# Performance work log

Measured on AMD Instinct MI355X. Metric: run time of the kernel, lower is better.

The kernel has to match this reference:

```python
import jax, jax.numpy as jnp
import numpy as np

K = 3          # kernel_size (cubic)
S = 1          # stride
N_ITER = 3     # routing_iter
LAMBDA = 0.01  # inverse temperature used in M-step (CapsLayer default)
EPS = 1e-9


def _space_to_batch(x, k, s):
    # x: [B, D, H, W, C, ...] -> [B, oD, oH, oW, k^3 * C, ...]
    # patch ordering (kd, kh, kw, c) matches CapsLayer's gather+transpose+reshape.
    B, D, H, W, C = x.shape[:5]
    trail = x.shape[5:]
    oD = (D - k) // s + 1
    oH = (H - k) // s + 1
    oW = (W - k) // s + 1
    blocks = []
    for kd in range(k):
        for kh in range(k):
            for kw in range(k):
                blocks.append(x[:, kd:kd + oD * s:s, kh:kh + oH * s:s, kw:kw + oW * s:s])
    p = jnp.stack(blocks, axis=4)  # [B,oD,oH,oW,k^3,C,...]
    return p.reshape((B, oD, oH, oW, k ** 3 * C) + trail)


def _lse(x, axis):
    return jax.scipy.special.logsumexp(x, axis=axis, keepdims=True)


def _m_step(log_R, log_act, vote, bv, ba):
    # log_R: [...,I,O,1], log_act: [...,I,1,1], vote: [...,I,O,P]
    log_Ra = log_R + log_act
    R_sum = jnp.sum(jnp.exp(log_Ra), axis=-3, keepdims=True)        # [...,1,O,1]
    log_nR = log_Ra - _lse(log_Ra, axis=-3)                          # [...,I,O,1]
    pose = jnp.sum(vote * jnp.exp(log_nR), axis=-3, keepdims=True)   # [...,1,O,P]
    log_var = _lse(log_nR + jnp.log(jnp.square(vote - pose) + EPS), axis=-3)
    cost = R_sum * (bv + 0.5 * log_var)                              # [...,1,O,P]
    logit = LAMBDA * (ba - jnp.sum(cost, axis=-1, keepdims=True))    # [...,1,O,1]
    return pose, log_var, jax.nn.log_sigmoid(logit)


def _e_step(pose, log_var, log_act_out, vote):
    # per-dim Gaussian log-likelihood of votes under (pose, var)
    lp = -0.5 * (jnp.square(vote - pose) / jnp.exp(log_var) + log_var + jnp.log(2.0 * jnp.pi))
    lp = jnp.sum(lp, axis=-1, keepdims=True)                         # [...,I,O,1]
    logit = log_act_out + lp
    return logit - _lse(logit, axis=-2)                              # softmax over O


def _forward(pose, activation, W, beta_v, beta_a):
    pb = _space_to_batch(pose, K, S)            # [B,oD,oH,oW,I,4,4]
    ab = _space_to_batch(activation, K, S)      # [B,oD,oH,oW,I]
    # votes: W[i,o] @ pose_patch[...,i] -> [B,oD,oH,oW,I,O,4,4]
    vote = jnp.einsum('iork,bdhwikc->bdhwiorc', W, pb)
    vs = vote.shape
    vote = vote.reshape(vs[:-2] + (vs[-2] * vs[-1],))   # [...,I,O,16]
    nO = vote.shape[-2]
    log_act = jnp.log(ab + EPS)[..., None, None]        # [...,I,1,1]
    log_R = jnp.full(vote.shape[:-1] + (1,), -jnp.log(float(nO)), vote.dtype)
    bv = beta_v[None, None, None, None, None, :, :]     # [1,1,1,1,1,O,1]
    ba = beta_a[None, None, None, None, None, :, :]
    for t in range(N_ITER):
        v = vote if t == N_ITER - 1 else jax.lax.stop_gradient(vote)
        p, log_var, log_a = _m_step(log_R, log_act, v, bv, ba)
        if t < N_ITER - 1:
            log_R = _e_step(p, log_var, log_a, jax.lax.stop_gradient(vote))
    out_pose = jnp.squeeze(p, axis=-3).reshape(vs[:4] + (vs[-3], vs[-2], vs[-1]))  # [B,oD,oH,oW,O,4,4]
    out_act = jnp.exp(jnp.squeeze(log_a, axis=(-3, -1)))                            # [B,oD,oH,oW,O]
    return out_pose, out_act


def setup_inputs() -> dict:
    key = jax.random.key(0)
    k1, k2, k3, k4, k5 = jax.random.split(key, 5)
    pose = jax.random.normal(k1, (1, 12, 12, 12, 8, 4, 4), dtype=jnp.float32)
    activation = jax.random.uniform(k2, (1, 12, 12, 12, 8), dtype=jnp.float32)
    W = jax.random.normal(k3, (216, 16, 4, 4), dtype=jnp.float32)
    beta_v = jax.random.normal(k4, (16, 1), dtype=jnp.float32)
    beta_a = jax.random.normal(k5, (16, 1), dtype=jnp.float32)
    return {"pose": pose, "activation": activation, "W": W, "beta_v": beta_v, "beta_a": beta_a}


def reference(pose, activation, W, beta_v, beta_a):
    return _forward(pose, activation, W, beta_v, beta_a)
```

## Files before the change

kernel.cpp:

```cpp
#include <hip/hip_runtime.h>

#define NITER 3
#define LAMBDA 0.01f
#define EPS 1e-9f
#define LOG2PI 1.8378770664093453f

#define DIN 12
#define CIN 8
#define NI 216
#define NO 16
#define PPAD 20
#define RSTR 216

__global__ __launch_bounds__(512, 2)
void caps_em_kernel(const float* __restrict__ pose,
                    const float* __restrict__ act,
                    const float* __restrict__ W,
                    const float* __restrict__ beta_v,
                    const float* __restrict__ beta_a,
                    float* __restrict__ out)
{
    __shared__ __align__(16) float sPT[NI][PPAD];
    __shared__ __align__(16) float sRaT[NO][RSTR];
    __shared__ float sAct[NI];
    __shared__ __align__(16) float sPoseM[NO][16];
    __shared__ __align__(16) float sIvM[NO][16];
    __shared__ float sCo[NO];

    const int t = threadIdx.x;
    const int b = blockIdx.x;
    const int od = b / 100;
    const int rem = b - od * 100;
    const int oh = rem / 10;
    const int ow = rem - oh * 10;

    const int o = t >> 5;
    const int j = t & 31;

    for (int u = t; u < NI * 4; u += 512) {
        int i = u >> 2, q = u & 3;
        int ci = i & 7, n = i >> 3;
        int kw = n % 3, n2 = n / 3;
        int kh = n2 % 3, kd = n2 / 3;
        const float4 v = *(const float4*)&pose[((((od + kd) * DIN + (oh + kh)) * DIN + (ow + kw)) * CIN + ci) * 16 + q * 4];
        sPT[i][0 + q]  = v.x;
        sPT[i][4 + q]  = v.y;
        sPT[i][8 + q]  = v.z;
        sPT[i][12 + q] = v.w;
    }
    if (t < NI) {
        int i = t;
        int ci = i & 7, n = i >> 3;
        int kw = n % 3, n2 = n / 3;
        int kh = n2 % 3, kd = n2 / 3;
        sAct[i] = act[(((od + kd) * DIN + (oh + kh)) * DIN + (ow + kw)) * CIN + ci] + EPS;
    }

    const float4* W4 = (const float4*)W;
    float4 wreg[7][4];
#pragma unroll
    for (int k = 0; k < 7; ++k) {
        const int iw = min(j + 32 * k, NI - 1);
        const float4* Wp = W4 + (iw * 16 + o) * 4;
        wreg[k][0] = Wp[0];
        wreg[k][1] = Wp[1];
        wreg[k][2] = Wp[2];
        wreg[k][3] = Wp[3];
    }
    const float bv_o = beta_v[o];
    const float ba_o = beta_a[o];
    __syncthreads();

    const int b4 = (j >> 4) & 1, b3 = (j >> 3) & 1, b2 = (j >> 2) & 1, b1 = (j >> 1) & 1;
    const bool lastPartial = (j >= 24);

    for (int it = 0; it < NITER; ++it) {
        float m1[16], m2[16];
#pragma unroll
        for (int q = 0; q < 16; ++q) { m1[q] = 0.f; m2[q] = 0.f; }
        float rs = 0.f;
#pragma unroll
        for (int k = 0; k < 7; ++k) {
            const int i = j + 32 * k;
            const int ip = min(i, NI - 1);
            float ra = (it == 0) ? sAct[ip] * 0.0625f : sRaT[o][ip];
            if (k == 6 && lastPartial) ra = 0.f;
            rs += ra;
#pragma unroll
            for (int cc = 0; cc < 4; ++cc) {
                const float4 pt = *(const float4*)&sPT[ip][cc * 4];
#pragma unroll
                for (int rr = 0; rr < 4; ++rr) {
                    float v = wreg[k][rr].x * pt.x;
                    v = fmaf(wreg[k][rr].y, pt.y, v);
                    v = fmaf(wreg[k][rr].z, pt.z, v);
                    v = fmaf(wreg[k][rr].w, pt.w, v);
                    m1[rr * 4 + cc] = fmaf(ra, v, m1[rr * 4 + cc]);
                    m2[rr * 4 + cc] = fmaf(ra * v, v, m2[rr * 4 + cc]);
                }
            }
        }

#pragma unroll
        for (int q = 0; q < 8; ++q) {
            float s1 = b4 ? m1[q] : m1[q + 8];
            float s2 = b4 ? m2[q] : m2[q + 8];
            m1[q] = (b4 ? m1[q + 8] : m1[q]) + __shfl_xor(s1, 16);
            m2[q] = (b4 ? m2[q + 8] : m2[q]) + __shfl_xor(s2, 16);
        }
#pragma unroll
        for (int q = 0; q < 4; ++q) {
            float s1 = b3 ? m1[q] : m1[q + 4];
            float s2 = b3 ? m2[q] : m2[q + 4];
            m1[q] = (b3 ? m1[q + 4] : m1[q]) + __shfl_xor(s1, 8);
            m2[q] = (b3 ? m2[q + 4] : m2[q]) + __shfl_xor(s2, 8);
        }
#pragma unroll
        for (int q = 0; q < 2; ++q) {
            float s1 = b2 ? m1[q] : m1[q + 2];
            float s2 = b2 ? m2[q] : m2[q + 2];
            m1[q] = (b2 ? m1[q + 2] : m1[q]) + __shfl_xor(s1, 4);
            m2[q] = (b2 ? m2[q + 2] : m2[q]) + __shfl_xor(s2, 4);
        }
        {
            float s1 = b1 ? m1[0] : m1[1];
            float s2 = b1 ? m2[0] : m2[1];
            m1[0] = (b1 ? m1[1] : m1[0]) + __shfl_xor(s1, 2);
            m2[0] = (b1 ? m2[1] : m2[0]) + __shfl_xor(s2, 2);
        }
        m1[0] += __shfl_xor(m1[0], 1);
        m2[0] += __shfl_xor(m2[0], 1);
        rs += __shfl_xor(rs, 16);
        rs += __shfl_xor(rs, 8);
        rs += __shfl_xor(rs, 4);
        rs += __shfl_xor(rs, 2);
        rs += __shfl_xor(rs, 1);
        const int e = j >> 1;

        const float inv_rs = 1.0f / rs;
        const float pe = m1[0] * inv_rs;
        const float ve = fmaxf(m2[0] * inv_rs - pe * pe, 0.0f) + EPS;
        const float lv = __logf(ve);

        float SL = lv;
        SL += __shfl_xor(SL, 1);
        SL += __shfl_xor(SL, 2);
        SL += __shfl_xor(SL, 4);
        SL += __shfl_xor(SL, 8);
        SL += __shfl_xor(SL, 16);
        SL *= 0.5f;

        const float cost  = rs * (16.0f * bv_o + 0.5f * SL);
        const float logit = LAMBDA * (ba_o - cost);

        if (it == NITER - 1) {
            if ((j & 1) == 0) out[(b * NO + o) * 16 + e] = pe;
            if (j == 0) out[256000 + b * NO + o] = 1.0f / (1.0f + __expf(-logit));
            return;
        }

        const float log_a = (logit >= 0.0f) ? -log1pf(__expf(-logit))
                                            : logit - log1pf(__expf(logit));
        if ((j & 1) == 0) {
            sPoseM[o][e] = pe;
            sIvM[o][e]   = 1.0f / ve;
        }
        if (j == 0) sCo[o] = log_a - 0.5f * SL - 8.0f * LOG2PI;
        __syncthreads();

        {
            float pv[16], iv16[16];
            *(float4*)&pv[0]    = *(const float4*)&sPoseM[o][0];
            *(float4*)&pv[4]    = *(const float4*)&sPoseM[o][4];
            *(float4*)&pv[8]    = *(const float4*)&sPoseM[o][8];
            *(float4*)&pv[12]   = *(const float4*)&sPoseM[o][12];
            *(float4*)&iv16[0]  = *(const float4*)&sIvM[o][0];
            *(float4*)&iv16[4]  = *(const float4*)&sIvM[o][4];
            *(float4*)&iv16[8]  = *(const float4*)&sIvM[o][8];
            *(float4*)&iv16[12] = *(const float4*)&sIvM[o][12];
            const float Co = sCo[o];
#pragma unroll
            for (int k = 0; k < 7; ++k) {
                const int i = j + 32 * k;
                const int ip = min(i, NI - 1);
                float q = 0.f;
#pragma unroll
                for (int cc = 0; cc < 4; ++cc) {
                    const float4 pt = *(const float4*)&sPT[ip][cc * 4];
#pragma unroll
                    for (int rr = 0; rr < 4; ++rr) {
                        float v = wreg[k][rr].x * pt.x;
                        v = fmaf(wreg[k][rr].y, pt.y, v);
                        v = fmaf(wreg[k][rr].z, pt.z, v);
                        v = fmaf(wreg[k][rr].w, pt.w, v);
                        const float d = v - pv[rr * 4 + cc];
                        q = fmaf(d * d, iv16[rr * 4 + cc], q);
                    }
                }
                if (!(k == 6 && lastPartial)) {
                    sRaT[o][i] = Co - 0.5f * q;
                }
            }
        }
        __syncthreads();

        if (t < NI) {
            float l[16];
            float mx = -1e30f;
#pragma unroll
            for (int oo = 0; oo < 16; ++oo) { l[oo] = sRaT[oo][t]; mx = fmaxf(mx, l[oo]); }
            float s = 0.f;
#pragma unroll
            for (int oo = 0; oo < 16; ++oo) { l[oo] = __expf(l[oo] - mx); s += l[oo]; }
            const float sc = sAct[t] / s;
#pragma unroll
            for (int oo = 0; oo < 16; ++oo) sRaT[oo][t] = sc * l[oo];
        }
        __syncthreads();
    }
}

extern "C" void kernel_launch(void* const* d_in, const int* in_sizes, int n_in,
                              void* d_out, int out_size, void* d_ws, size_t ws_size,
                              hipStream_t stream) {
    const float* pose = (const float*)d_in[0];
    const float* actv = (const float*)d_in[1];
    const float* W    = (const float*)d_in[2];
    const float* bv   = (const float*)d_in[3];
    const float* ba   = (const float*)d_in[4];
    float* out = (float*)d_out;
    caps_em_kernel<<<dim3(1000), dim3(512), 0, stream>>>(pose, actv, W, bv, ba, out);
}
```

Measured before the change: 146.8 us.

## Precompute votes once into registers instead of recomputing each routing pass

Computes all 7x16 vote values per thread once after loading, holding them in registers (112 floats), and reuses them in every M-step and E-step instead of recomputing W·pose from shared memory each pass. W loads are moved before the pose staging so the global loads overlap. Occupancy is pinned at 2 waves per EU to allow the larger register footprint. This removes repeated FMA and LDS traffic, at the cost of high VGPR pressure and possible spills.

Result: faster. 131.9 us (-10.2%).

```diff
diff --git a/kernel.cpp b/kernel.cpp
--- a/kernel.cpp
+++ b/kernel.cpp
@@ -12,7 +12,7 @@
 #define PPAD 20
 #define RSTR 216
 
-__global__ __launch_bounds__(512, 2)
+__global__ __launch_bounds__(512) __attribute__((amdgpu_waves_per_eu(2, 2)))
 void caps_em_kernel(const float* __restrict__ pose,
                     const float* __restrict__ act,
                     const float* __restrict__ W,
@@ -37,6 +37,18 @@
     const int o = t >> 5;
     const int j = t & 31;
 
+    const float4* W4 = (const float4*)W;
+    float4 w[7][4];
+#pragma unroll
+    for (int k = 0; k < 7; ++k) {
+        const int iw = min(j + 32 * k, NI - 1);
+        const float4* Wp = W4 + (iw * 16 + o) * 4;
+        w[k][0] = Wp[0];
+        w[k][1] = Wp[1];
+        w[k][2] = Wp[2];
+        w[k][3] = Wp[3];
+    }
+
     for (int u = t; u < NI * 4; u += 512) {
         int i = u >> 2, q = u & 3;
         int ci = i & 7, n = i >> 3;
@@ -55,22 +67,28 @@
         int kh = n2 % 3, kd = n2 / 3;
         sAct[i] = act[(((od + kd) * DIN + (oh + kh)) * DIN + (ow + kw)) * CIN + ci] + EPS;
     }
-
-    const float4* W4 = (const float4*)W;
-    float4 wreg[7][4];
-#pragma unroll
-    for (int k = 0; k < 7; ++k) {
-        const int iw = min(j + 32 * k, NI - 1);
-        const float4* Wp = W4 + (iw * 16 + o) * 4;
-        wreg[k][0] = Wp[0];
-        wreg[k][1] = Wp[1];
-        wreg[k][2] = Wp[2];
-        wreg[k][3] = Wp[3];
-    }
     const float bv_o = beta_v[o];
     const float ba_o = beta_a[o];
     __syncthreads();
 
+    float vo[7][16];
+#pragma unroll
+    for (int k = 0; k < 7; ++k) {
+        const int ip = min(j + 32 * k, NI - 1);
+#pragma unroll
+        for (int cc = 0; cc < 4; ++cc) {
+            const float4 pt = *(const float4*)&sPT[ip][cc * 4];
+#pragma unroll
+            for (int rr = 0; rr < 4; ++rr) {
+                float v = w[k][rr].x * pt.x;
+                v = fmaf(w[k][rr].y, pt.y, v);
+                v = fmaf(w[k][rr].z, pt.z, v);
+                v = fmaf(w[k][rr].w, pt.w, v);
+                vo[k][rr * 4 + cc] = v;
+            }
+        }
+    }
+
     const int b4 = (j >> 4) & 1, b3 = (j >> 3) & 1, b2 = (j >> 2) & 1, b1 = (j >> 1) & 1;
     const bool lastPartial = (j >= 24);
 
@@ -81,23 +99,16 @@
         float rs = 0.f;
 #pragma unroll
         for (int k = 0; k < 7; ++k) {
-            const int i = j + 32 * k;
-            const int ip = min(i, NI - 1);
+            const int ip = min(j + 32 * k, NI - 1);
             float ra = (it == 0) ? sAct[ip] * 0.0625f : sRaT[o][ip];
             if (k == 6 && lastPartial) ra = 0.f;
             rs += ra;
 #pragma unroll
-            for (int cc = 0; cc < 4; ++cc) {
-                const float4 pt = *(const float4*)&sPT[ip][cc * 4];
-#pragma unroll
-                for (int rr = 0; rr < 4; ++rr) {
-                    float v = wreg[k][rr].x * pt.x;
-                    v = fmaf(wreg[k][rr].y, pt.y, v);
-                    v = fmaf(wreg[k][rr].z, pt.z, v);
-                    v = fmaf(wreg[k][rr].w, pt.w, v);
-                    m1[rr * 4 + cc] = fmaf(ra, v, m1[rr * 4 + cc]);
-                    m2[rr * 4 + cc] = fmaf(ra * v, v, m2[rr * 4 + cc]);
-                }
+            for (int q = 0; q < 16; ++q) {
+                const float v  = vo[k][q];
+                const float rv = ra * v;
+                m1[q] += rv;
+                m2[q] = fmaf(rv, v, m2[q]);
             }
         }
 
@@ -182,20 +193,11 @@
 #pragma unroll
             for (int k = 0; k < 7; ++k) {
                 const int i = j + 32 * k;
-                const int ip = min(i, NI - 1);
                 float q = 0.f;
 #pragma unroll
-                for (int cc = 0; cc < 4; ++cc) {
-                    const float4 pt = *(const float4*)&sPT[ip][cc * 4];
-#pragma unroll
-                    for (int rr = 0; rr < 4; ++rr) {
-                        float v = wreg[k][rr].x * pt.x;
-                        v = fmaf(wreg[k][rr].y, pt.y, v);
-                        v = fmaf(wreg[k][rr].z, pt.z, v);
-                        v = fmaf(wreg[k][rr].w, pt.w, v);
-                        const float d = v - pv[rr * 4 + cc];
-                        q = fmaf(d * d, iv16[rr * 4 + cc], q);
-                    }
+                for (int qq = 0; qq < 16; ++qq) {
+                    const float d = vo[k][qq] - pv[qq];
+                    q = fmaf(d * d, iv16[qq], q);
                 }
                 if (!(k == 6 && lastPartial)) {
                     sRaT[o][i] = Co - 0.5f * q;
```
